# Kernel optimization log

Hardware: AMD Instinct MI355X
Metric: run time of the kernel (lower is better)

The kernel has to match this reference:

```python
import jax, jax.numpy as jnp
import numpy as np

KERNEL = 8
WEIGHT_INIT = np.array([0.49403, -0.44625, 0.82544, 0.99267, 1.6915, -2.0835, 2.9114,
                        -5.6555, 3.5984, -10.205, 20.828, -0.0022237, 0.0097854, 157.35],
                       dtype=np.float32)


def setup_inputs() -> dict:
    key = jax.random.key(0)
    x = jax.random.normal(key, (2048, 128, KERNEL, KERNEL), dtype=jnp.float32)
    weight = jnp.asarray(WEIGHT_INIT)
    return {"input": x, "weight": weight}


def reference(input, weight):
    eye = jnp.eye(KERNEL, dtype=input.dtype)  # serves as both mask and eye(8)
    # A = I - x @ x^T  over trailing two dims
    A = eye - jnp.matmul(input, jnp.swapaxes(input, 2, 3))
    B = jnp.matmul(A, A)
    C = jnp.matmul(B, A)
    D = jnp.matmul(C, A)
    E = jnp.matmul(D, A)
    F = jnp.matmul(E, A)
    G = jnp.matmul(F, A)
    Mat = (weight[0] * A + weight[1] * B + weight[2] * C + weight[3] * D
           + weight[4] * E + weight[5] * F + weight[6] * G + weight[7] * eye)
    return input + jnp.matmul(Mat, input)
```

## Files before the change

### kernel.cpp

```cpp
#include <hip/hip_runtime.h>


typedef float v2f __attribute__((ext_vector_type(2)));

__device__ __forceinline__ v2f pk_mul(v2f a, v2f b) {
    v2f d;
    asm("v_pk_mul_f32 %0, %1, %2" : "=v"(d) : "v"(a), "v"(b));
    return d;
}
__device__ __forceinline__ void pk_fma(v2f &acc, v2f a, v2f b) {
    asm("v_pk_fma_f32 %0, %1, %2, %0" : "+v"(acc) : "v"(a), "v"(b));
}
__device__ __forceinline__ v2f pk_mul_lo(v2f a, v2f b) {
    v2f d;
    asm("v_pk_mul_f32 %0, %1, %2 op_sel:[0,0] op_sel_hi:[0,1]"
        : "=v"(d) : "v"(a), "v"(b));
    return d;
}
__device__ __forceinline__ void pk_fma_lo(v2f &acc, v2f a, v2f b) {
    asm("v_pk_fma_f32 %0, %1, %2, %0 op_sel:[0,0,0] op_sel_hi:[0,1,1]"
        : "+v"(acc) : "v"(a), "v"(b));
}
__device__ __forceinline__ void pk_fma_hi(v2f &acc, v2f a, v2f b) {
    asm("v_pk_fma_f32 %0, %1, %2, %0 op_sel:[1,0,0] op_sel_hi:[1,1,1]"
        : "+v"(acc) : "v"(a), "v"(b));
}

__device__ __forceinline__ float pswap(float x)
{
    return __builtin_bit_cast(float,
        __builtin_amdgcn_update_dpp(0, __builtin_bit_cast(int, x),
                                    0xB1, 0xF, 0xF, true));
}

#define GLOAD_LDS16(gp, lp)                                               \
    __builtin_amdgcn_global_load_lds(                                     \
        (const __attribute__((address_space(1))) void*)(gp),              \
        (__attribute__((address_space(3))) void*)(lp), 16, 0, 0)

#define AE(p, q) A[(p) < (q) ? (p) : (q)][(p) < (q) ? (q) : (p)]

#define POW_STEP(wk)                                                      \
    {                                                                     \
        const v2f wv = (v2f){(wk), (wk)};                                 \
        _Pragma("unroll")                                                 \
        for (int j = 0; j < 2; ++j) {                                     \
            v2f n[8];                                                     \
            _Pragma("unroll")                                             \
            for (int p = 0; p < 8; ++p) {                                 \
                v2f a = pk_mul_lo(Ar[p][0], y[j][0]);                     \
                pk_fma_hi(a, Ar[p][0], y[j][1]);                          \
                pk_fma_lo(a, Ar[p][1], y[j][2]);                          \
                pk_fma_hi(a, Ar[p][1], y[j][3]);                          \
                pk_fma_lo(a, Ar[p][2], y[j][4]);                          \
                pk_fma_hi(a, Ar[p][2], y[j][5]);                          \
                pk_fma_lo(a, Ar[p][3], y[j][6]);                          \
                pk_fma_hi(a, Ar[p][3], y[j][7]);                          \
                n[p] = a;                                                 \
            }                                                             \
            _Pragma("unroll")                                             \
            for (int p = 0; p < 8; ++p) {                                 \
                y[j][p] = n[p];                                           \
                pk_fma(acc[j][p], wv, n[p]);                              \
            }                                                             \
        }                                                                 \
    }

__global__ __launch_bounds__(256, 2)
void ns_poly_kernel(const float* __restrict__ in,
                    const float* __restrict__ wp,
                    float* __restrict__ out)
{
    __shared__ float4 lds[2048];

    const int tid  = threadIdx.x;
    const int wave = tid >> 6;
    const int lane = tid & 63;
    const int l    = lane >> 1;
    const int h    = lane & 1;

    const float w0 = wp[0], w1 = wp[1], w2 = wp[2], w3 = wp[3];
    const float w4 = wp[4], w5 = wp[5], w6 = wp[6], w7 = wp[7];

    float4* L = lds + wave * 512;

    const size_t base =
        ((size_t)blockIdx.x * 128 + (size_t)wave * 32) * 16;
    const float4* __restrict__ gin  = reinterpret_cast<const float4*>(in);
    float4*       __restrict__ gout = reinterpret_cast<float4*>(out);

#pragma unroll
    for (int it = 0; it < 8; ++it) {
        const int C = it * 64 + lane;
        const int Cs = C ^ (((C >> 4) & 3) << 1);
        GLOAD_LDS16(gin + base + Cs, L + it * 64);
    }
    asm volatile("s_waitcnt vmcnt(0)" ::: "memory");
    __builtin_amdgcn_sched_barrier(0);

    v2f y[2][8];
#pragma unroll
    for (int g = 0; g < 8; ++g) {
        const int f4 = (l * 16 + g * 2 + h) ^ ((l & 3) << 1);
        const float4 v = L[f4];
        y[0][g] = (v2f){v.x, v.y};
        y[1][g] = (v2f){v.z, v.w};
    }

    float S[8][8];
#pragma unroll
    for (int p = 0; p < 8; ++p)
#pragma unroll
        for (int q = p; q < 8; ++q) {
            v2f a = pk_mul(y[0][p], y[0][q]);
            pk_fma(a, y[1][p], y[1][q]);
            S[p][q] = a.x + a.y;
        }

    float A[8][8];
#pragma unroll
    for (int p = 0; p < 8; ++p)
#pragma unroll
        for (int q = p; q < 8; ++q) {
            const float other = pswap(S[p][q]);
            A[p][q] = (p == q ? 1.0f : 0.0f) - S[p][q] - other;
        }

    v2f Ar[8][4];
#pragma unroll
    for (int p = 0; p < 8; ++p)
#pragma unroll
        for (int jq = 0; jq < 4; ++jq)
            Ar[p][jq] = (v2f){AE(p, 2 * jq), AE(p, 2 * jq + 1)};

    v2f acc[2][8];
    const v2f w7v = (v2f){1.0f + w7, 1.0f + w7};
#pragma unroll
    for (int j = 0; j < 2; ++j)
#pragma unroll
        for (int p = 0; p < 8; ++p)
            acc[j][p] = pk_mul(w7v, y[j][p]);

    POW_STEP(w0);
    POW_STEP(w1);
    POW_STEP(w2);
    POW_STEP(w3);
    POW_STEP(w4);
    POW_STEP(w5);
    POW_STEP(w6);

#pragma unroll
    for (int g = 0; g < 8; ++g) {
        const int f4 = (l * 16 + g * 2 + h) ^ ((l & 3) << 1);
        L[f4] = make_float4(acc[0][g].x, acc[0][g].y,
                            acc[1][g].x, acc[1][g].y);
    }
    asm volatile("s_waitcnt lgkmcnt(0)" ::: "memory");

#pragma unroll
    for (int it = 0; it < 8; ++it) {
        const int C = it * 64 + lane;
        gout[base + C] = L[C ^ (((C >> 4) & 3) << 1)];
    }
}

extern "C" void kernel_launch(void* const* d_in, const int* in_sizes, int n_in,
                              void* d_out, int out_size, void* d_ws, size_t ws_size,
                              hipStream_t stream)
{
    const float* in = (const float*)d_in[0];
    const float* w  = (const float*)d_in[1];
    float* outp     = (float*)d_out;

    const int nmat   = in_sizes[0] / 64;
    const int blocks = nmat / 128;
    ns_poly_kernel<<<blocks, 256, 0, stream>>>(in, w, outp);
}
```

Baseline: 119.6 us.

## Split each matrix across four lanes instead of two

Each 8x8 matrix is now handled by four lanes, each owning two columns, where before two lanes each owned four. The Gram-matrix reduction now takes two DPP swaps, and blocks handle 64 matrices instead of 128, doubling the grid and halving LDS per block. This halves per-thread register state (y, acc), which could raise occupancy and parallelism. In exchange, every lane redundantly computes the symmetric A matrix and the power-step matrix-vector work, so total ALU work per matrix roughly doubles.

```diff
diff --git a/kernel.cpp b/kernel.cpp
--- a/kernel.cpp
+++ b/kernel.cpp
@@ -26,11 +26,17 @@
         : "+v"(acc) : "v"(a), "v"(b));
 }
 
-__device__ __forceinline__ float pswap(float x)
+__device__ __forceinline__ float qswap1(float x)
 {
     return __builtin_bit_cast(float,
         __builtin_amdgcn_update_dpp(0, __builtin_bit_cast(int, x),
                                     0xB1, 0xF, 0xF, true));
+}
+__device__ __forceinline__ float qswap2(float x)
+{
+    return __builtin_bit_cast(float,
+        __builtin_amdgcn_update_dpp(0, __builtin_bit_cast(int, x),
+                                    0x4E, 0xF, 0xF, true));
 }
 
 #define GLOAD_LDS16(gp, lp)                                               \
@@ -43,26 +49,23 @@
 #define POW_STEP(wk)                                                      \
     {                                                                     \
         const v2f wv = (v2f){(wk), (wk)};                                 \
+        v2f n[8];                                                         \
         _Pragma("unroll")                                                 \
-        for (int j = 0; j < 2; ++j) {                                     \
-            v2f n[8];                                                     \
-            _Pragma("unroll")                                             \
-            for (int p = 0; p < 8; ++p) {                                 \
-                v2f a = pk_mul_lo(Ar[p][0], y[j][0]);                     \
-                pk_fma_hi(a, Ar[p][0], y[j][1]);                          \
-                pk_fma_lo(a, Ar[p][1], y[j][2]);                          \
-                pk_fma_hi(a, Ar[p][1], y[j][3]);                          \
-                pk_fma_lo(a, Ar[p][2], y[j][4]);                          \
-                pk_fma_hi(a, Ar[p][2], y[j][5]);                          \
-                pk_fma_lo(a, Ar[p][3], y[j][6]);                          \
-                pk_fma_hi(a, Ar[p][3], y[j][7]);                          \
-                n[p] = a;                                                 \
-            }                                                             \
-            _Pragma("unroll")                                             \
-            for (int p = 0; p < 8; ++p) {                                 \
-                y[j][p] = n[p];                                           \
-                pk_fma(acc[j][p], wv, n[p]);                              \
-            }                                                             \
+        for (int p = 0; p < 8; ++p) {                                     \
+            v2f a = pk_mul_lo(Ar[p][0], y[0]);                            \
+            pk_fma_hi(a, Ar[p][0], y[1]);                                 \
+            pk_fma_lo(a, Ar[p][1], y[2]);                                 \
+            pk_fma_hi(a, Ar[p][1], y[3]);                                 \
+            pk_fma_lo(a, Ar[p][2], y[4]);                                 \
+            pk_fma_hi(a, Ar[p][2], y[5]);                                 \
+            pk_fma_lo(a, Ar[p][3], y[6]);                                 \
+            pk_fma_hi(a, Ar[p][3], y[7]);                                 \
+            n[p] = a;                                                     \
+        }                                                                 \
+        _Pragma("unroll")                                                 \
+        for (int p = 0; p < 8; ++p) {                                     \
+            y[p] = n[p];                                                  \
+            pk_fma(acc[p], wv, n[p]);                                     \
         }                                                                 \
     }
 
@@ -71,40 +74,42 @@
                     const float* __restrict__ wp,
                     float* __restrict__ out)
 {
-    __shared__ float4 lds[2048];
+    __shared__ float4 lds[1024];
 
     const int tid  = threadIdx.x;
     const int wave = tid >> 6;
     const int lane = tid & 63;
-    const int l    = lane >> 1;
-    const int h    = lane & 1;
+    const int l    = lane >> 2;
+    const int j    = lane & 3;
+    const int hj   = j >> 1;
+    const int bh   = j & 1;
 
     const float w0 = wp[0], w1 = wp[1], w2 = wp[2], w3 = wp[3];
     const float w4 = wp[4], w5 = wp[5], w6 = wp[6], w7 = wp[7];
 
-    float4* L = lds + wave * 512;
+    float4* L  = lds + wave * 256;
+    float2* L2 = reinterpret_cast<float2*>(L);
 
     const size_t base =
-        ((size_t)blockIdx.x * 128 + (size_t)wave * 32) * 16;
+        ((size_t)blockIdx.x * 64 + (size_t)wave * 16) * 16;
     const float4* __restrict__ gin  = reinterpret_cast<const float4*>(in);
     float4*       __restrict__ gout = reinterpret_cast<float4*>(out);
 
 #pragma unroll
-    for (int it = 0; it < 8; ++it) {
-        const int C = it * 64 + lane;
+    for (int it = 0; it < 4; ++it) {
+        const int C  = it * 64 + lane;
         const int Cs = C ^ (((C >> 4) & 3) << 1);
         GLOAD_LDS16(gin + base + Cs, L + it * 64);
     }
     asm volatile("s_waitcnt vmcnt(0)" ::: "memory");
     __builtin_amdgcn_sched_barrier(0);
 
-    v2f y[2][8];
+    v2f y[8];
 #pragma unroll
     for (int g = 0; g < 8; ++g) {
-        const int f4 = (l * 16 + g * 2 + h) ^ ((l & 3) << 1);
-        const float4 v = L[f4];
-        y[0][g] = (v2f){v.x, v.y};
-        y[1][g] = (v2f){v.z, v.w};
+        const int idx2 = (((l * 16 + g * 2 + hj) ^ ((l & 3) << 1)) << 1) | bh;
+        const float2 v = L2[idx2];
+        y[g] = (v2f){v.x, v.y};
     }
 
     float S[8][8];
@@ -112,8 +117,7 @@
     for (int p = 0; p < 8; ++p)
 #pragma unroll
         for (int q = p; q < 8; ++q) {
-            v2f a = pk_mul(y[0][p], y[0][q]);
-            pk_fma(a, y[1][p], y[1][q]);
+            const v2f a = pk_mul(y[p], y[q]);
             S[p][q] = a.x + a.y;
         }
 
@@ -122,8 +126,9 @@
     for (int p = 0; p < 8; ++p)
 #pragma unroll
         for (int q = p; q < 8; ++q) {
-            const float other = pswap(S[p][q]);
-            A[p][q] = (p == q ? 1.0f : 0.0f) - S[p][q] - other;
+            const float r    = S[p][q] + qswap1(S[p][q]);
+            const float full = r + qswap2(r);
+            A[p][q] = (p == q ? 1.0f : 0.0f) - full;
         }
 
     v2f Ar[8][4];
@@ -133,13 +138,11 @@
         for (int jq = 0; jq < 4; ++jq)
             Ar[p][jq] = (v2f){AE(p, 2 * jq), AE(p, 2 * jq + 1)};
 
-    v2f acc[2][8];
+    v2f acc[8];
     const v2f w7v = (v2f){1.0f + w7, 1.0f + w7};
 #pragma unroll
-    for (int j = 0; j < 2; ++j)
-#pragma unroll
-        for (int p = 0; p < 8; ++p)
-            acc[j][p] = pk_mul(w7v, y[j][p]);
+    for (int p = 0; p < 8; ++p)
+        acc[p] = pk_mul(w7v, y[p]);
 
     POW_STEP(w0);
     POW_STEP(w1);
@@ -151,14 +154,13 @@
 
 #pragma unroll
     for (int g = 0; g < 8; ++g) {
-        const int f4 = (l * 16 + g * 2 + h) ^ ((l & 3) << 1);
-        L[f4] = make_float4(acc[0][g].x, acc[0][g].y,
-                            acc[1][g].x, acc[1][g].y);
+        const int idx2 = (((l * 16 + g * 2 + hj) ^ ((l & 3) << 1)) << 1) | bh;
+        L2[idx2] = make_float2(acc[g].x, acc[g].y);
     }
     asm volatile("s_waitcnt lgkmcnt(0)" ::: "memory");
 
 #pragma unroll
-    for (int it = 0; it < 8; ++it) {
+    for (int it = 0; it < 4; ++it) {
         const int C = it * 64 + lane;
         gout[base + C] = L[C ^ (((C >> 4) & 3) << 1)];
     }
@@ -173,6 +175,6 @@
     float* outp     = (float*)d_out;
 
     const int nmat   = in_sizes[0] / 64;
-    const int blocks = nmat / 128;
+    const int blocks = nmat / 64;
     ns_poly_kernel<<<blocks, 256, 0, stream>>>(in, w, outp);
 }
```

After: 121.0 us. No clear change (+1.2%).
